# Kernel tuning notes

Hardware: AMD Instinct MI355X
Metric: run time of the kernel (lower is better)

Reference implementation:

```python
import jax, jax.numpy as jnp
import numpy as np

ALPHA = 0.2  # LeakyReLU negative slope
NEG_BIG = -9e15


def setup_inputs() -> dict:
    key = jax.random.key(0)
    k1, k2, k3, k4 = jax.random.split(key, 4)
    B, N, F_in, F_out = 8, 2048, 256, 256
    x = jax.random.normal(k1, (B, N, F_in), dtype=jnp.float32)
    adj = jax.random.randint(k2, (B, N, N), 0, 2, dtype=jnp.int32)
    # Xavier-uniform init like nn.init.xavier_uniform_
    limW = float(np.sqrt(6.0 / (F_in + F_out)))
    W = jax.random.uniform(k3, (F_in, F_out), minval=-limW, maxval=limW, dtype=jnp.float32)
    lima = float(np.sqrt(6.0 / (2 * F_out + 1)))
    a = jax.random.uniform(k4, (2 * F_out, 1), minval=-lima, maxval=lima, dtype=jnp.float32)
    return {"x": x, "adj": adj, "W": W, "a": a}


def reference(x, adj, W, a):
    # x: (B,N,Fin), adj: (B,N,N), W: (Fin,Fout), a: (2*Fout,1)
    F_out = W.shape[1]
    Wh = jnp.einsum('bnf,fo->bno', x, W)            # (B,N,Fout)
    a1, a2 = a[:F_out, 0], a[F_out:, 0]
    # e[b,i,j] = leakyrelu(Wh[b,i]@a1 + Wh[b,j]@a2)  (equivalent to concat+matmul)
    e = (Wh @ a1)[:, :, None] + (Wh @ a2)[:, None, :]  # (B,N,N)
    e = jnp.where(e > 0, e, ALPHA * e)
    attention = jnp.where(adj > 0, e, NEG_BIG)
    attention = jax.nn.softmax(attention, axis=-1)
    # dropout is identity in eval mode (training=False)
    h_prime = jnp.einsum('bij,bjo->bio', attention, Wh)  # (B,N,Fout)
    return jax.nn.elu(h_prime)  # concat=True -> ELU
```

## Files before the change

### kernel.cpp

```cpp
#include <hip/hip_runtime.h>
#include <hip/hip_fp16.h>

typedef _Float16 f16;
typedef _Float16 half4 __attribute__((ext_vector_type(4)));
typedef _Float16 half8 __attribute__((ext_vector_type(8)));
typedef float f32x4 __attribute__((ext_vector_type(4)));

#define BATCH 8
#define NTOK 2048
#define FIN 256
#define FOUT 256
#define ALPHA 0.2f
#define LOG2E 1.44269504088896340736f


__device__ __forceinline__ void gload16(const void* g, void* l) {
    __builtin_amdgcn_global_load_lds(
        (const __attribute__((address_space(1))) unsigned int*)(g),
        (__attribute__((address_space(3))) unsigned int*)(l), 16, 0, 0);
}

__global__ void k_wt(const float* __restrict__ W, f16* __restrict__ WT) {
    __shared__ float t[32][33];
    int o0 = blockIdx.x * 32, k0 = blockIdx.y * 32;
    int tx = threadIdx.x, ty = threadIdx.y;
    t[ty][tx] = W[(k0 + ty) * FOUT + o0 + tx];
    __syncthreads();
    WT[(o0 + ty) * FIN + (k0 + tx)] = (f16)t[tx][ty];
}

__global__ __launch_bounds__(256) void k_gemm(const float* __restrict__ x,
                                              const f16* __restrict__ WT,
                                              const float* __restrict__ a,
                                              f16* __restrict__ WhT,
                                              float* __restrict__ s1,
                                              float* __restrict__ s2) {
    __shared__ __align__(16) char gsmem[46080];
    int t = threadIdx.x;
    int lane = t & 63, w = t >> 6;
    f16* Ah = (f16*)gsmem;
    f16* Bt = (f16*)(gsmem + 9216);
    int m0 = blockIdx.x * 64;
    int lr = lane & 15, lg = lane >> 4;
    f32x4 acc[4][4] = {};

    for (int k0 = 0; k0 < FIN; k0 += 64) {
        {
            int r = t >> 2, c = (t & 3) * 16;
            const float* src = x + (size_t)(m0 + r) * FIN + k0 + c;
            f32x4 v0 = *(const f32x4*)(src);
            f32x4 v1 = *(const f32x4*)(src + 4);
            f32x4 v2 = *(const f32x4*)(src + 8);
            f32x4 v3 = *(const f32x4*)(src + 12);
            half8 h0, h1;
#pragma unroll
            for (int q = 0; q < 4; q++) {
                h0[q] = (f16)v0[q]; h0[q + 4] = (f16)v1[q];
                h1[q] = (f16)v2[q]; h1[q + 4] = (f16)v3[q];
            }
            f16* dst = Ah + r * 72 + c;
            *(half8*)dst = h0;
            *(half8*)(dst + 8) = h1;
        }
        {
            const f16* src = WT + (size_t)t * FIN + k0;
            f16* dst = Bt + t * 72;
#pragma unroll
            for (int q = 0; q < 8; q++)
                *(half8*)(dst + q * 8) = *(const half8*)(src + q * 8);
        }
        __syncthreads();
#pragma unroll
        for (int kc = 0; kc < 2; kc++) {
            int krow = kc * 32 + lg * 8;
            half8 af[4], bf[4];
#pragma unroll
            for (int fi = 0; fi < 4; fi++)
                af[fi] = *(half8*)(Ah + (fi * 16 + lr) * 72 + krow);
#pragma unroll
            for (int fo = 0; fo < 4; fo++)
                bf[fo] = *(half8*)(Bt + (w * 64 + fo * 16 + lr) * 72 + krow);
#pragma unroll
            for (int fi = 0; fi < 4; fi++)
#pragma unroll
                for (int fo = 0; fo < 4; fo++)
                    acc[fi][fo] = __builtin_amdgcn_mfma_f32_16x16x32_f16(
                        af[fi], bf[fo], acc[fi][fo], 0, 0, 0);
        }
        __syncthreads();
    }

    int b = m0 >> 11;
    int slab_i = (m0 & (NTOK - 1)) >> 6;
    int nbase = m0 & (NTOK - 1);

    float* sred = (float*)gsmem;
    f16* slab = (f16*)(gsmem + 9216);
    float a1v[4], a2v[4];
#pragma unroll
    for (int fo = 0; fo < 4; fo++) {
        int o = w * 64 + fo * 16 + lr;
        a1v[fo] = a[o];
        a2v[fo] = a[FOUT + o];
    }
#pragma unroll
    for (int fi = 0; fi < 4; fi++) {
        f32x4 p1 = {}, p2 = {};
#pragma unroll
        for (int fo = 0; fo < 4; fo++) {
            p1 += acc[fi][fo] * a1v[fo];
            p2 += acc[fi][fo] * a2v[fo];
        }
#pragma unroll
        for (int q = 0; q < 4; q++) {
#pragma unroll
            for (int d = 1; d < 16; d <<= 1) {
                p1[q] += __shfl_xor(p1[q], d);
                p2[q] += __shfl_xor(p2[q], d);
            }
        }
        if (lr == 0) {
            int row = fi * 16 + lg * 4;
#pragma unroll
            for (int q = 0; q < 4; q++) {
                sred[w * 64 + row + q] = p1[q];
                sred[256 + w * 64 + row + q] = p2[q];
            }
        }
    }
#pragma unroll
    for (int fi = 0; fi < 4; fi++) {
        int jg8 = fi * 2 + (lg >> 1), jq0 = (lg & 1) * 4;
#pragma unroll
        for (int fo = 0; fo < 4; fo++) {
            int o = w * 64 + fo * 16 + lr;
            half4 hv;
#pragma unroll
            for (int q = 0; q < 4; q++) hv[q] = (f16)acc[fi][fo][q];
            *(half4*)(slab + o * 64 + ((jg8 ^ (o & 7)) * 8) + jq0) = hv;
        }
    }
    __syncthreads();

    if (t < 64) {
        s1[(size_t)b * NTOK + nbase + t] =
            sred[t] + sred[64 + t] + sred[128 + t] + sred[192 + t];
    } else if (t < 128) {
        int r2 = t - 64;
        s2[(size_t)b * NTOK + nbase + r2] =
            sred[256 + r2] + sred[320 + r2] + sred[384 + r2] + sred[448 + r2];
    }
    {
        const int4* sl = (const int4*)slab;
        int4* gd = (int4*)(WhT + ((size_t)(b * 32 + slab_i) * 256) * 64);
#pragma unroll
        for (int i = 0; i < 8; i++) gd[i * 256 + t] = sl[i * 256 + t];
    }
}

__global__ __launch_bounds__(512, 1) void k_attn(const int* __restrict__ adj,
                                                 const f16* __restrict__ WhT,
                                                 const float* __restrict__ s1g,
                                                 const float* __restrict__ s2g,
                                                 float* __restrict__ out) {
    __shared__ __align__(16) char smem[107296];
    f16* Bl = (f16*)smem;
    float* s2_lds = (float*)(smem + 65536);
    unsigned* mask_lds = (unsigned*)(smem + 73728);
    f16* P_lds = (f16*)(smem + 90624);
    float* l_lds = (float*)(smem + 107008);
    float* wmax = (float*)(smem + 107264);

    int b = blockIdx.x & 7;
    int i0 = (blockIdx.x >> 3) * 64;
    int t = threadIdx.x;
    int lane = t & 63, w = t >> 6;
    int lr = lane & 15, lg = lane >> 4;
    int oq = w & 3, rg = w >> 2;
    int r4 = lane >> 3, j8 = lane & 7;
    int srow = w * 8 + r4;

    {
        f32x4 sv4 = ((const f32x4*)(s2g + (size_t)b * NTOK))[t];
        sv4 = sv4 * LOG2E;
        ((f32x4*)s2_lds)[t] = sv4;
        float tmx = fmaxf(fmaxf(sv4[0], sv4[1]), fmaxf(sv4[2], sv4[3]));
#pragma unroll
        for (int d = 1; d < 64; d <<= 1) tmx = fmaxf(tmx, __shfl_xor(tmx, d));
        if (lane == 0) wmax[w] = tmx;
    }

    const char* wsrc = (const char*)WhT + (size_t)b * (32 * 32768);
    {
        const char* s0 = wsrc + w * 4096 + lane * 16;
        char* d0 = (char*)Bl + w * 4096;
#pragma unroll
        for (int k = 0; k < 4; k++) gload16(s0 + k * 1024, d0 + k * 1024);
        const char* s1p = wsrc + 32768 + w * 4096 + lane * 16;
        char* d1 = (char*)Bl + 32768 + w * 4096;
#pragma unroll
        for (int k = 0; k < 4; k++) gload16(s1p + k * 1024, d1 + k * 1024);
    }

    {
        const int4* abase = (const int4*)(adj + ((size_t)(b * NTOK + i0 + w * 8)) * NTOK)
                            + lane * 8;
        int4 c0[8], c1[8];
#pragma unroll
        for (int k = 0; k < 8; k++) { c0[k] = abase[k]; c1[k] = abase[512 + k]; }
        for (int rp = 0; rp < 4; rp++) {
            int4 n0[8], n1[8];
            if (rp < 3) {
#pragma unroll
                for (int k = 0; k < 8; k++) {
                    n0[k] = abase[(2 * rp + 2) * 512 + k];
                    n1[k] = abase[(2 * rp + 3) * 512 + k];
                }
            }
            unsigned m0 = 0, m1 = 0;
#pragma unroll
            for (int k = 0; k < 8; k++) {
                m0 |= (unsigned)(c0[k].x > 0) << (k * 4);
                m0 |= (unsigned)(c0[k].y > 0) << (k * 4 + 1);
                m0 |= (unsigned)(c0[k].z > 0) << (k * 4 + 2);
                m0 |= (unsigned)(c0[k].w > 0) << (k * 4 + 3);
                m1 |= (unsigned)(c1[k].x > 0) << (k * 4);
                m1 |= (unsigned)(c1[k].y > 0) << (k * 4 + 1);
                m1 |= (unsigned)(c1[k].z > 0) << (k * 4 + 2);
                m1 |= (unsigned)(c1[k].w > 0) << (k * 4 + 3);
            }
            mask_lds[(w * 8 + 2 * rp) * 66 + lane] = m0;
            mask_lds[(w * 8 + 2 * rp + 1) * 66 + lane] = m1;
#pragma unroll
            for (int k = 0; k < 8; k++) { c0[k] = n0[k]; c1[k] = n1[k]; }
        }
    }

    float s1r = s1g[(size_t)b * NTOK + i0 + srow] * LOG2E;
    float l_acc = 0.f;

    __syncthreads();

    float s2m = wmax[0];
#pragma unroll
    for (int k = 1; k < 8; k++) s2m = fmaxf(s2m, wmax[k]);
    float txr = s1r + s2m;
    float mxr = fmaxf(txr, ALPHA * txr);

    f32x4 acc[2][4] = {};

    for (int s = 0; s < 32; s++) {
        int buf = s & 1;
        {
            unsigned mw = mask_lds[srow * 66 + s * 2 + (j8 >> 2)];
            unsigned bits = (mw >> ((j8 & 3) * 8)) & 0xffu;
            f32x4 sA = *(const f32x4*)&s2_lds[s * 64 + j8 * 8];
            f32x4 sB = *(const f32x4*)&s2_lds[s * 64 + j8 * 8 + 4];
            half8 ph;
#pragma unroll
            for (int q = 0; q < 8; q++) {
                float sv = q < 4 ? sA[q] : sB[q - 4];
                float sx = s1r + sv;
                float ev = fmaxf(sx, ALPHA * sx);
                float p = ((bits >> q) & 1) ? exp2f(ev - mxr) : 0.f;
                l_acc += p;
                ph[q] = (f16)p;
            }
            *(half8*)&P_lds[buf * 4096 + srow * 64 + ((j8 ^ (srow & 7)) * 8)] = ph;
        }
        __syncthreads();

        {
            const f16* Pb = P_lds + buf * 4096;
            const f16* Bb = Bl + buf * 16384;
            half8 af[2][2];
#pragma unroll
            for (int fi = 0; fi < 2; fi++)
#pragma unroll
                for (int kc = 0; kc < 2; kc++) {
                    int ra = rg * 32 + fi * 16 + lr;
                    af[fi][kc] = *(const half8*)&Pb[ra * 64 + (((kc * 4 + lg) ^ (ra & 7)) * 8)];
                }
#pragma unroll
            for (int ot = 0; ot < 4; ot++) {
                int o = oq * 64 + ot * 16 + lr;
#pragma unroll
                for (int kc = 0; kc < 2; kc++) {
                    half8 bf = *(const half8*)&Bb[o * 64 + (((kc * 4 + lg) ^ (o & 7)) * 8)];
                    acc[0][ot] = __builtin_amdgcn_mfma_f32_16x16x32_f16(af[0][kc], bf, acc[0][ot], 0, 0, 0);
                    acc[1][ot] = __builtin_amdgcn_mfma_f32_16x16x32_f16(af[1][kc], bf, acc[1][ot], 0, 0, 0);
                }
            }
        }
        __syncthreads();

        if (s < 30) {
            const char* src = wsrc + (size_t)(s + 2) * 32768 + w * 4096 + lane * 16;
            char* dst = (char*)Bl + buf * 32768 + w * 4096;
#pragma unroll
            for (int k = 0; k < 4; k++) gload16(src + k * 1024, dst + k * 1024);
        }
    }

    l_acc += __shfl_xor(l_acc, 1);
    l_acc += __shfl_xor(l_acc, 2);
    l_acc += __shfl_xor(l_acc, 4);
    if (j8 == 0) l_lds[srow] = l_acc;
    __syncthreads();

    f32x4 rl0, rl1;
#pragma unroll
    for (int q = 0; q < 4; q++) {
        rl0[q] = 1.f / l_lds[rg * 32 + lg * 4 + q];
        rl1[q] = 1.f / l_lds[rg * 32 + 16 + lg * 4 + q];
    }
#pragma unroll
    for (int ot = 0; ot < 4; ot++) {
        int o = oq * 64 + ot * 16 + lr;
#pragma unroll
        for (int q = 0; q < 4; q++) {
            int ra = rg * 32 + lg * 4 + q;
            float u = acc[0][ot][q] * rl0[q];
            u = u > 0.f ? u : __expf(u) - 1.f;
            __builtin_nontemporal_store(u, &out[((size_t)(b * NTOK + i0 + ra)) * FOUT + o]);
            int rb = ra + 16;
            float v = acc[1][ot][q] * rl1[q];
            v = v > 0.f ? v : __expf(v) - 1.f;
            __builtin_nontemporal_store(v, &out[((size_t)(b * NTOK + i0 + rb)) * FOUT + o]);
        }
    }
}

extern "C" void kernel_launch(void* const* d_in, const int* in_sizes, int n_in,
                              void* d_out, int out_size, void* d_ws, size_t ws_size,
                              hipStream_t stream) {
    const float* x = (const float*)d_in[0];
    const int* adj = (const int*)d_in[1];
    const float* W = (const float*)d_in[2];
    const float* a = (const float*)d_in[3];
    float* out = (float*)d_out;

    char* ws = (char*)d_ws;
    f16* WT = (f16*)ws;
    f16* WhT = (f16*)(ws + 131072);
    float* s1 = (float*)(ws + 131072 + 8388608);
    float* s2 = s1 + BATCH * NTOK;

    k_wt<<<dim3(FOUT / 32, FIN / 32), dim3(32, 32), 0, stream>>>(W, WT);
    k_gemm<<<dim3(BATCH * NTOK / 64), 256, 0, stream>>>(x, WT, a, WhT, s1, s2);
    k_attn<<<dim3(BATCH * NTOK / 64), 512, 0, stream>>>(adj, WhT, s1, s2, out);
}
```

Baseline: 83.05 us.

## Halve attention row tile and stage WhT through registers for higher occupancy

The attention kernel now handles 32 query rows per block instead of 64. The launch grid doubles and LDS use per block drops to about half, so up to four blocks can be resident. The async global-to-LDS double buffer for WhT is replaced by a single LDS buffer fed from a register-prefetched next stage. This aims to improve latency hiding for the adjacency stream and spread work across more CUs. In exchange, every block re-reads the full per-batch WhT, so total L2 traffic for WhT doubles, and each block issues fewer MFMAs per barrier.

```diff
diff --git a/kernel.cpp b/kernel.cpp
--- a/kernel.cpp
+++ b/kernel.cpp
@@ -13,12 +13,6 @@
 #define ALPHA 0.2f
 #define LOG2E 1.44269504088896340736f
 
-
-__device__ __forceinline__ void gload16(const void* g, void* l) {
-    __builtin_amdgcn_global_load_lds(
-        (const __attribute__((address_space(1))) unsigned int*)(g),
-        (__attribute__((address_space(3))) unsigned int*)(l), 16, 0, 0);
-}
 
 __global__ void k_wt(const float* __restrict__ W, f16* __restrict__ WT) {
     __shared__ float t[32][33];
@@ -158,27 +152,26 @@
     }
 }
 
-__global__ __launch_bounds__(512, 1) void k_attn(const int* __restrict__ adj,
+__global__ __launch_bounds__(512, 4) void k_attn(const int* __restrict__ adj,
                                                  const f16* __restrict__ WhT,
                                                  const float* __restrict__ s1g,
                                                  const float* __restrict__ s2g,
                                                  float* __restrict__ out) {
-    __shared__ __align__(16) char smem[107296];
+    __shared__ __align__(16) char smem[53664];
     f16* Bl = (f16*)smem;
-    float* s2_lds = (float*)(smem + 65536);
-    unsigned* mask_lds = (unsigned*)(smem + 73728);
-    f16* P_lds = (f16*)(smem + 90624);
-    float* l_lds = (float*)(smem + 107008);
-    float* wmax = (float*)(smem + 107264);
+    float* s2_lds = (float*)(smem + 32768);
+    unsigned* mask_lds = (unsigned*)(smem + 40960);
+    char* P_b = smem + 49408;
+    float* l_lds = (float*)(smem + 53504);
+    float* wmax = (float*)(smem + 53632);
 
     int b = blockIdx.x & 7;
-    int i0 = (blockIdx.x >> 3) * 64;
+    int i0 = (blockIdx.x >> 3) * 32;
     int t = threadIdx.x;
     int lane = t & 63, w = t >> 6;
     int lr = lane & 15, lg = lane >> 4;
-    int oq = w & 3, rg = w >> 2;
-    int r4 = lane >> 3, j8 = lane & 7;
-    int srow = w * 8 + r4;
+    int r4 = lane >> 4, jg = lane & 15;
+    int srow = w * 4 + r4;
 
     {
         f32x4 sv4 = ((const f32x4*)(s2g + (size_t)b * NTOK))[t];
@@ -191,49 +184,45 @@
     }
 
     const char* wsrc = (const char*)WhT + (size_t)b * (32 * 32768);
-    {
-        const char* s0 = wsrc + w * 4096 + lane * 16;
-        char* d0 = (char*)Bl + w * 4096;
-#pragma unroll
-        for (int k = 0; k < 4; k++) gload16(s0 + k * 1024, d0 + k * 1024);
-        const char* s1p = wsrc + 32768 + w * 4096 + lane * 16;
-        char* d1 = (char*)Bl + 32768 + w * 4096;
-#pragma unroll
-        for (int k = 0; k < 4; k++) gload16(s1p + k * 1024, d1 + k * 1024);
-    }
-
-    {
-        const int4* abase = (const int4*)(adj + ((size_t)(b * NTOK + i0 + w * 8)) * NTOK)
+    int4 st[4];
+    {
+        const int4* p = (const int4*)(wsrc + t * 16);
+        st[0] = p[0]; st[1] = p[512]; st[2] = p[1024]; st[3] = p[1536];
+    }
+
+    {
+        const int4* abase = (const int4*)(adj + ((size_t)(b * NTOK + i0 + w * 4)) * NTOK)
                             + lane * 8;
-        int4 c0[8], c1[8];
-#pragma unroll
-        for (int k = 0; k < 8; k++) { c0[k] = abase[k]; c1[k] = abase[512 + k]; }
-        for (int rp = 0; rp < 4; rp++) {
-            int4 n0[8], n1[8];
-            if (rp < 3) {
-#pragma unroll
-                for (int k = 0; k < 8; k++) {
-                    n0[k] = abase[(2 * rp + 2) * 512 + k];
-                    n1[k] = abase[(2 * rp + 3) * 512 + k];
-                }
-            }
-            unsigned m0 = 0, m1 = 0;
+        int4 cur[8], nxt[8];
+#pragma unroll
+        for (int k = 0; k < 8; k++) cur[k] = abase[k];
+        for (int r = 0; r < 4; r++) {
+            if (r < 3) {
+#pragma unroll
+                for (int k = 0; k < 8; k++) nxt[k] = abase[(r + 1) * 512 + k];
+            } else {
+#pragma unroll
+                for (int k = 0; k < 8; k++) nxt[k] = cur[k];
+            }
+            unsigned m = 0;
 #pragma unroll
             for (int k = 0; k < 8; k++) {
-                m0 |= (unsigned)(c0[k].x > 0) << (k * 4);
-                m0 |= (unsigned)(c0[k].y > 0) << (k * 4 + 1);
-                m0 |= (unsigned)(c0[k].z > 0) << (k * 4 + 2);
-                m0 |= (unsigned)(c0[k].w > 0) << (k * 4 + 3);
-                m1 |= (unsigned)(c1[k].x > 0) << (k * 4);
-                m1 |= (unsigned)(c1[k].y > 0) << (k * 4 + 1);
-                m1 |= (unsigned)(c1[k].z > 0) << (k * 4 + 2);
-                m1 |= (unsigned)(c1[k].w > 0) << (k * 4 + 3);
-            }
-            mask_lds[(w * 8 + 2 * rp) * 66 + lane] = m0;
-            mask_lds[(w * 8 + 2 * rp + 1) * 66 + lane] = m1;
-#pragma unroll
-            for (int k = 0; k < 8; k++) { c0[k] = n0[k]; c1[k] = n1[k]; }
-        }
+                m |= (unsigned)(cur[k].x > 0) << (k * 4);
+                m |= (unsigned)(cur[k].y > 0) << (k * 4 + 1);
+                m |= (unsigned)(cur[k].z > 0) << (k * 4 + 2);
+                m |= (unsigned)(cur[k].w > 0) << (k * 4 + 3);
+            }
+            mask_lds[(w * 4 + r) * 66 + lane] = m;
+#pragma unroll
+            for (int k = 0; k < 8; k++) cur[k] = nxt[k];
+        }
+    }
+
+    {
+        int4* q = (int4*)(smem + t * 16);
+        q[0] = st[0]; q[512] = st[1]; q[1024] = st[2]; q[1536] = st[3];
+        const int4* p = (const int4*)(wsrc + 32768 + t * 16);
+        st[0] = p[0]; st[1] = p[512]; st[2] = p[1024]; st[3] = p[1536];
     }
 
     float s1r = s1g[(size_t)b * NTOK + i0 + srow] * LOG2E;
@@ -247,46 +236,41 @@
     float txr = s1r + s2m;
     float mxr = fmaxf(txr, ALPHA * txr);
 
-    f32x4 acc[2][4] = {};
+    f32x4 acc[2][2] = {};
 
     for (int s = 0; s < 32; s++) {
-        int buf = s & 1;
         {
-            unsigned mw = mask_lds[srow * 66 + s * 2 + (j8 >> 2)];
-            unsigned bits = (mw >> ((j8 & 3) * 8)) & 0xffu;
-            f32x4 sA = *(const f32x4*)&s2_lds[s * 64 + j8 * 8];
-            f32x4 sB = *(const f32x4*)&s2_lds[s * 64 + j8 * 8 + 4];
-            half8 ph;
-#pragma unroll
-            for (int q = 0; q < 8; q++) {
-                float sv = q < 4 ? sA[q] : sB[q - 4];
-                float sx = s1r + sv;
+            unsigned word = mask_lds[srow * 66 + s * 2 + (jg >> 3)];
+            unsigned bits = (word >> ((jg & 7) * 4)) & 0xfu;
+            f32x4 sA = *(const f32x4*)&s2_lds[s * 64 + jg * 4];
+            half4 ph;
+#pragma unroll
+            for (int q = 0; q < 4; q++) {
+                float sx = s1r + sA[q];
                 float ev = fmaxf(sx, ALPHA * sx);
                 float p = ((bits >> q) & 1) ? exp2f(ev - mxr) : 0.f;
                 l_acc += p;
                 ph[q] = (f16)p;
             }
-            *(half8*)&P_lds[buf * 4096 + srow * 64 + ((j8 ^ (srow & 7)) * 8)] = ph;
+            *(half4*)(P_b + srow * 128 + (((jg >> 1) ^ (srow & 7)) * 16) + (jg & 1) * 8) = ph;
         }
         __syncthreads();
 
         {
-            const f16* Pb = P_lds + buf * 4096;
-            const f16* Bb = Bl + buf * 16384;
             half8 af[2][2];
 #pragma unroll
             for (int fi = 0; fi < 2; fi++)
 #pragma unroll
                 for (int kc = 0; kc < 2; kc++) {
-                    int ra = rg * 32 + fi * 16 + lr;
-                    af[fi][kc] = *(const half8*)&Pb[ra * 64 + (((kc * 4 + lg) ^ (ra & 7)) * 8)];
+                    int ra = fi * 16 + lr;
+                    af[fi][kc] = *(const half8*)(P_b + ra * 128 + (((kc * 4 + lg) ^ (ra & 7)) * 16));
                 }
 #pragma unroll
-            for (int ot = 0; ot < 4; ot++) {
-                int o = oq * 64 + ot * 16 + lr;
+            for (int ot = 0; ot < 2; ot++) {
+                int o = w * 32 + ot * 16 + lr;
 #pragma unroll
                 for (int kc = 0; kc < 2; kc++) {
-                    half8 bf = *(const half8*)&Bb[o * 64 + (((kc * 4 + lg) ^ (o & 7)) * 8)];
+                    half8 bf = *(const half8*)((char*)Bl + o * 128 + (((kc * 4 + lg) ^ (o & 7)) * 16));
                     acc[0][ot] = __builtin_amdgcn_mfma_f32_16x16x32_f16(af[0][kc], bf, acc[0][ot], 0, 0, 0);
                     acc[1][ot] = __builtin_amdgcn_mfma_f32_16x16x32_f16(af[1][kc], bf, acc[1][ot], 0, 0, 0);
                 }
@@ -294,36 +278,39 @@
         }
         __syncthreads();
 
-        if (s < 30) {
-            const char* src = wsrc + (size_t)(s + 2) * 32768 + w * 4096 + lane * 16;
-            char* dst = (char*)Bl + buf * 32768 + w * 4096;
-#pragma unroll
-            for (int k = 0; k < 4; k++) gload16(src + k * 1024, dst + k * 1024);
+        if (s < 31) {
+            int4* q = (int4*)(smem + t * 16);
+            q[0] = st[0]; q[512] = st[1]; q[1024] = st[2]; q[1536] = st[3];
+            if (s < 30) {
+                const int4* p = (const int4*)(wsrc + (size_t)(s + 2) * 32768 + t * 16);
+                st[0] = p[0]; st[1] = p[512]; st[2] = p[1024]; st[3] = p[1536];
+            }
         }
     }
 
     l_acc += __shfl_xor(l_acc, 1);
     l_acc += __shfl_xor(l_acc, 2);
     l_acc += __shfl_xor(l_acc, 4);
-    if (j8 == 0) l_lds[srow] = l_acc;
+    l_acc += __shfl_xor(l_acc, 8);
+    if (jg == 0) l_lds[srow] = l_acc;
     __syncthreads();
 
     f32x4 rl0, rl1;
 #pragma unroll
     for (int q = 0; q < 4; q++) {
-        rl0[q] = 1.f / l_lds[rg * 32 + lg * 4 + q];
-        rl1[q] = 1.f / l_lds[rg * 32 + 16 + lg * 4 + q];
-    }
-#pragma unroll
-    for (int ot = 0; ot < 4; ot++) {
-        int o = oq * 64 + ot * 16 + lr;
+        rl0[q] = 1.f / l_lds[lg * 4 + q];
+        rl1[q] = 1.f / l_lds[16 + lg * 4 + q];
+    }
+#pragma unroll
+    for (int ot = 0; ot < 2; ot++) {
+        int o = w * 32 + ot * 16 + lr;
 #pragma unroll
         for (int q = 0; q < 4; q++) {
-            int ra = rg * 32 + lg * 4 + q;
+            int ra = lg * 4 + q;
             float u = acc[0][ot][q] * rl0[q];
             u = u > 0.f ? u : __expf(u) - 1.f;
             __builtin_nontemporal_store(u, &out[((size_t)(b * NTOK + i0 + ra)) * FOUT + o]);
-            int rb = ra + 16;
+            int rb = 16 + lg * 4 + q;
             float v = acc[1][ot][q] * rl1[q];
             v = v > 0.f ? v : __expf(v) - 1.f;
             __builtin_nontemporal_store(v, &out[((size_t)(b * NTOK + i0 + rb)) * FOUT + o]);
@@ -348,5 +335,5 @@
 
     k_wt<<<dim3(FOUT / 32, FIN / 32), dim3(32, 32), 0, stream>>>(W, WT);
     k_gemm<<<dim3(BATCH * NTOK / 64), 256, 0, stream>>>(x, WT, a, WhT, s1, s2);
-    k_attn<<<dim3(BATCH * NTOK / 64), 512, 0, stream>>>(adj, WhT, s1, s2, out);
+    k_attn<<<dim3(BATCH * NTOK / 32), 512, 0, stream>>>(adj, WhT, s1, s2, out);
 }
```

After: 177.5 us. +113.7%, slower.
